# Kernel optimization log

Measured on AMD Instinct MI355X. Metric: run time of the kernel, lower is better.

The kernel has to match this reference:

```python
import jax, jax.numpy as jnp
import numpy as np

LN_EPS = 1e-5

def _layernorm(x, g, b):
    mu = x.mean(-1, keepdims=True)
    var = ((x - mu) ** 2).mean(-1, keepdims=True)
    return (x - mu) * jax.lax.rsqrt(var + LN_EPS) * g + b

def setup_inputs() -> dict:
    key = jax.random.key(0)
    ks = jax.random.split(key, 5)
    B, S, H, V = 1, 1024, 768, 50257
    return {
        "hidden_states": jax.random.normal(ks[0], (B, S, H), jnp.float32),
        "attention_mask": jnp.ones((B, S), jnp.int32),
        "alpha": jnp.float32(0.1),
        "ln_gamma": jnp.ones((H,), jnp.float32),
        "ln_beta": jnp.zeros((H,), jnp.float32),
        "W1": jax.random.normal(ks[1], (H, H), jnp.float32) * 0.02,
        "b1": jnp.zeros((H,), jnp.float32),
        "W2": jax.random.normal(ks[2], (H, H), jnp.float32) * 0.02,
        "b2": jnp.zeros((H,), jnp.float32),
        "lm_head_w": jax.random.normal(ks[3], (V, H), jnp.float32) * 0.02,
        "n_processors": 4,
        "k_steps": 4,
    }

def reference(hidden_states, attention_mask, alpha, ln_gamma, ln_beta,
              W1, b1, W2, b2, lm_head_w, n_processors, k_steps):
    P = int(n_processors)
    K = int(k_steps)
    mask = attention_mask.astype(hidden_states.dtype)[..., None]        # [B,S,1]
    # processor_states: [P,B,S,H] (all initialized to the same hidden state)
    states = jnp.broadcast_to(hidden_states[None], (P,) + hidden_states.shape)
    for _ in range(K):
        # eval mode: dropout=identity, no noise -> mutate == mask multiply
        mut = states * mask                                             # [P,B,S,H]
        if P > 1:
            # mean of other processors = (sum_all - self)/(P-1)
            observe = (mut.sum(0, keepdims=True) - mut) / (P - 1)
        else:
            observe = jnp.zeros_like(mut)
        merged = mut + alpha * observe
        normed = _layernorm(merged, ln_gamma, ln_beta)
        h = jax.nn.gelu(jnp.einsum('pbsh,ih->pbsi', normed, W1) + b1,
                        approximate=False)
        delta = jnp.einsum('pbsi,hi->pbsh', h, W2) + b2
        states = (mut + delta) * mask
    consensus = states.mean(0)                                          # [B,S,H]
    logits = jnp.einsum('bsh,vh->bsv', consensus, lm_head_w)            # [B,S,V]
    processor_logits = jnp.einsum('pbsh,vh->pbsv', states, lm_head_w)   # [P,B,S,V]
    return logits, processor_logits, states
```

## Files before the change

kernel.cpp:

```cpp
#include <hip/hip_runtime.h>
#include <hip/hip_bf16.h>
#include <math.h>

#define S_LEN 1024
#define HDIM  768
#define NPROC 4
#define VOCAB 50257
#define KSTEPS 4
#define LOOP_BLOCKS 96

typedef __attribute__((ext_vector_type(4))) float f32x4;
typedef __attribute__((ext_vector_type(8))) short bf16x8;
typedef __attribute__((ext_vector_type(4))) short short4v;

static __device__ __forceinline__ ushort f2bf(float f) {
  union { __hip_bfloat16 b; ushort u; } cv;
  cv.b = __float2bfloat16(f);
  return cv.u;
}

#define GLOAD16(gp, lp) __builtin_amdgcn_global_load_lds( \
    (const __attribute__((address_space(1))) unsigned int*)(gp), \
    (__attribute__((address_space(3))) unsigned int*)(lp), 16, 0, 0)

__global__ void prep_weights(const float* __restrict__ lmw, const float* __restrict__ W1,
                             const float* __restrict__ W2, ushort* __restrict__ lm_bf,
                             ushort* __restrict__ w1_bf, ushort* __restrict__ w2_bf) {
  const int LM4 = VOCAB * HDIM / 4;
  const int W4  = HDIM * HDIM / 4;
  const int LMB = (LM4 + 255) / 256;
  const int WB  = (W4 + 255) / 256;
  const int bid = blockIdx.x;
  const float* in; ushort* out; int n4, i;
  if (bid < LMB)           { in = lmw; out = lm_bf; n4 = LM4; i = bid * 256 + threadIdx.x; }
  else if (bid < LMB + WB) { in = W1;  out = w1_bf; n4 = W4;  i = (bid - LMB) * 256 + threadIdx.x; }
  else                     { in = W2;  out = w2_bf; n4 = W4;  i = (bid - LMB - WB) * 256 + threadIdx.x; }
  if (i >= n4) return;
  f32x4 v = ((const f32x4*)in)[i];
  short4v o;
#pragma unroll
  for (int j = 0; j < 4; j++) o[j] = (short)f2bf(v[j]);
  ((short4v*)out)[i] = o;
}

__global__ __launch_bounds__(256) void bcast_logits(
    const float* __restrict__ src, float* __restrict__ dst) {
  const size_t n4 = (size_t)S_LEN * VOCAB / 4;
  for (size_t i = (size_t)blockIdx.x * 256 + threadIdx.x; i < n4;
       i += (size_t)gridDim.x * 256) {
    f32x4 v = ((const f32x4*)src)[i];
#pragma unroll
    for (int p = 0; p < NPROC; p++)
      ((f32x4*)dst)[(size_t)p * n4 + i] = v;
  }
}

static __device__ __forceinline__ void grid_barrier(int* cnt, int target) {
  __syncthreads();
  if (threadIdx.x == 0) {
    __threadfence();
    atomicAdd(cnt, 1);
    while (atomicAdd(cnt, 0) < target) { }
    __threadfence();
  }
  __syncthreads();
}

template <int MODE>
static __device__ __forceinline__ void mlp_phase(
    const ushort* __restrict__ A, const ushort* __restrict__ B,
    const float* __restrict__ bias, ushort* __restrict__ out_bf,
    const float* __restrict__ src, float* __restrict__ dst,
    const int* __restrict__ mask,
    ushort lsA[][4096], ushort lsB[][2048]) {
  const int tid = threadIdx.x;
  const int bx = blockIdx.x;
  const int mt = bx & 7;
  const int nt = bx >> 3;
  const int wv = tid >> 6, lane = tid & 63;
  const int wm = wv >> 1, wn = wv & 1;
  const int g = lane >> 4, lr = lane & 15;

  f32x4 acc[4][2];
#pragma unroll
  for (int i = 0; i < 4; i++)
#pragma unroll
    for (int j = 0; j < 2; j++) acc[i][j] = (f32x4){0.f, 0.f, 0.f, 0.f};

  const int koff = (tid & 3) * 8;
  const int arow0 = mt * 128 + (tid >> 2);
  const ushort* gA0 = A + (size_t)arow0 * HDIM + koff;
  const ushort* gA1 = gA0 + (size_t)64 * HDIM;
  const ushort* gB0 = B + (size_t)(nt * 64 + (tid >> 2)) * HDIM + koff;
  const int dstl = (tid >> 2) * 32 + (tid & 3) * 8;

#define STAGE(kt, buf) do {                      \
    const int o_ = (kt) * 32;                    \
    GLOAD16(gA0 + o_, &lsA[buf][dstl]);          \
    GLOAD16(gA1 + o_, &lsA[buf][2048 + dstl]);   \
    GLOAD16(gB0 + o_, &lsB[buf][dstl]);          \
  } while (0)

  constexpr int NT = HDIM / 32;
  STAGE(0, 0);
  STAGE(1, 1);
  int cur = 0;
  for (int kt = 0; kt < NT; ++kt) {
    if (kt < NT - 1) asm volatile("s_waitcnt vmcnt(3)" ::: "memory");
    else             asm volatile("s_waitcnt vmcnt(0)" ::: "memory");
    __builtin_amdgcn_s_barrier();
    __builtin_amdgcn_sched_barrier(0);
    bf16x8 af[4], bfr[2];
#pragma unroll
    for (int mi = 0; mi < 4; mi++)
      af[mi] = *(const bf16x8*)(&lsA[cur][(wm * 64 + mi * 16 + lr) * 32 + g * 8]);
#pragma unroll
    for (int ni = 0; ni < 2; ni++)
      bfr[ni] = *(const bf16x8*)(&lsB[cur][(wn * 32 + ni * 16 + lr) * 32 + g * 8]);
    asm volatile("s_waitcnt lgkmcnt(0)" ::: "memory");
    __builtin_amdgcn_sched_barrier(0);
    __builtin_amdgcn_s_setprio(1);
#pragma unroll
    for (int mi = 0; mi < 4; mi++)
#pragma unroll
      for (int ni = 0; ni < 2; ni++)
        acc[mi][ni] = __builtin_amdgcn_mfma_f32_16x16x32_bf16(af[mi], bfr[ni], acc[mi][ni], 0, 0, 0);
    __builtin_amdgcn_s_setprio(0);
    __builtin_amdgcn_s_barrier();
    __builtin_amdgcn_sched_barrier(0);
    if (kt + 2 < NT) STAGE(kt + 2, cur);
    cur ^= 1;
  }
#undef STAGE

#pragma unroll
  for (int mi = 0; mi < 4; mi++) {
    const int mrow = mt * 128 + wm * 64 + mi * 16 + g * 4;
#pragma unroll
    for (int ni = 0; ni < 2; ni++) {
      const int ncol = nt * 64 + wn * 32 + ni * 16 + lr;
      const float bv = bias[ncol];
      if (MODE == 0) {
#pragma unroll
        for (int j = 0; j < 4; j++) {
          float x = acc[mi][ni][j] + bv;
          float ge = 0.5f * x * (1.f + erff(x * 0.70710678118654752f));
          out_bf[(size_t)(mrow + j) * HDIM + ncol] = f2bf(ge);
        }
      } else {
#pragma unroll
        for (int j = 0; j < 4; j++) {
          const int m = mrow + j;
          const float mk = (float)mask[m];
          const size_t idx = (size_t)m * HDIM + ncol;
          const float mut = src[idx] * mk;
          const float ns = (mut + acc[mi][ni][j] + bv) * mk;
          dst[idx] = ns;
          if (out_bf) out_bf[idx] = f2bf(ns);
        }
      }
    }
  }
}

__global__ __launch_bounds__(256) void fused_loop(
    const float* __restrict__ hidden, const int* __restrict__ mask,
    const float* __restrict__ alphap, const float* __restrict__ gamma,
    const float* __restrict__ beta,
    const ushort* __restrict__ w1, const float* __restrict__ b1,
    const ushort* __restrict__ w2, const float* __restrict__ b2,
    float* __restrict__ st1, ushort* __restrict__ nrm, ushort* __restrict__ hbuf,
    ushort* __restrict__ a_bf, float* __restrict__ states, int* __restrict__ cnt) {
  __shared__ __align__(16) ushort lsA[2][4096];
  __shared__ __align__(16) ushort lsB[2][2048];
  __shared__ float rs_[4], rq_[4];
  const int tid = threadIdx.x;
  const float a1 = 1.0f + alphap[0];
  int gen = 0;

  for (int k = 0; k < KSTEPS; k++) {
    const float* src = (k == 0) ? hidden : st1;
    for (int s = blockIdx.x; s < S_LEN; s += LOOP_BLOCKS) {
      const float mk = (float)mask[s];
      float merged[3];
      float lsum = 0.f, lsq = 0.f;
#pragma unroll
      for (int e = 0; e < 3; e++) {
        const int h = tid + e * 256;
        float mg = src[(size_t)s * HDIM + h] * mk * a1;
        merged[e] = mg;
        lsum += mg;
        lsq += mg * mg;
      }
#pragma unroll
      for (int off = 32; off > 0; off >>= 1) {
        lsum += __shfl_down(lsum, off, 64);
        lsq  += __shfl_down(lsq, off, 64);
      }
      const int wv = tid >> 6, ln = tid & 63;
      if (ln == 0) { rs_[wv] = lsum; rq_[wv] = lsq; }
      __syncthreads();
      const float ts = rs_[0] + rs_[1] + rs_[2] + rs_[3];
      const float tq = rq_[0] + rq_[1] + rq_[2] + rq_[3];
      const float mu = ts * (1.f / HDIM);
      const float var = tq * (1.f / HDIM) - mu * mu;
      const float rstd = rsqrtf(var + 1e-5f);
#pragma unroll
      for (int e = 0; e < 3; e++) {
        const int h = tid + e * 256;
        float nv = (merged[e] - mu) * rstd * gamma[h] + beta[h];
        nrm[(size_t)s * HDIM + h] = f2bf(nv);
      }
      __syncthreads();
    }
    grid_barrier(cnt, (++gen) * LOOP_BLOCKS);
    mlp_phase<0>(nrm, w1, b1, hbuf, nullptr, nullptr, mask, lsA, lsB);
    grid_barrier(cnt, (++gen) * LOOP_BLOCKS);
    mlp_phase<1>(hbuf, w2, b2, (k == KSTEPS - 1) ? a_bf : nullptr, src, st1, mask, lsA, lsB);
    grid_barrier(cnt, (++gen) * LOOP_BLOCKS);
  }
  for (int i = blockIdx.x * 256 + tid; i < S_LEN * HDIM / 4; i += LOOP_BLOCKS * 256) {
    f32x4 v = ((const f32x4*)st1)[i];
#pragma unroll
    for (int p = 0; p < NPROC; p++)
      ((f32x4*)states)[(size_t)p * (S_LEN * HDIM / 4) + i] = v;
  }
}

__global__ __launch_bounds__(512, 2) void gemm_lm(
    const ushort* __restrict__ A, const ushort* __restrict__ B,
    float* __restrict__ logits, int nrowsB) {
  __shared__ __align__(16) ushort lds[2][4][8192];
  ushort* ldsb = &lds[0][0][0];
  const int tid = threadIdx.x;
  const int bx = blockIdx.x;
  const int mt = bx & 3;
  const int nt = bx >> 2;
  const int wv = tid >> 6, lane = tid & 63;
  const int wm = wv >> 2, wn = wv & 3;
  const int g = lane >> 4, lr = lane & 15;

  f32x4 acc[8][4];
#pragma unroll
  for (int i = 0; i < 8; i++)
#pragma unroll
    for (int j = 0; j < 4; j++) acc[i][j] = (f32x4){0.f, 0.f, 0.f, 0.f};

  const ushort* gsrc[4][2];
#pragma unroll
  for (int j = 0; j < 2; j++) {
    const int c = j * 512 + wv * 64 + lane;
    const int qa = c >> 9, ra = (c >> 3) & 63, oa = (c & 7) ^ (ra & 7);
    gsrc[0][j] = A + (size_t)(mt * 256 + qa * 128 + ra) * HDIM + oa * 8;
    gsrc[1][j] = A + (size_t)(mt * 256 + qa * 128 + 64 + ra) * HDIM + oa * 8;
    const int qb = c >> 8, rb = (c >> 3) & 31, ob = (c & 7) ^ (rb & 7);
    int r2 = nt * 256 + qb * 64 + rb;      if (r2 >= nrowsB) r2 = nrowsB - 1;
    int r3 = nt * 256 + qb * 64 + 32 + rb; if (r3 >= nrowsB) r3 = nrowsB - 1;
    gsrc[2][j] = B + (size_t)r2 * HDIM + ob * 8;
    gsrc[3][j] = B + (size_t)r3 * HDIM + ob * 8;
  }
  const int a_lane = wm * 4096 + lr * 64;
  const int b_lane = wn * 2048 + lr * 64;
  int slot8[2];
  slot8[0] = ((0 + g) ^ (lr & 7)) * 8;
  slot8[1] = ((4 + g) ^ (lr & 7)) * 8;

#define STG(R_, tt_) do {                                                     \
    ushort* dst_ = ldsb + (size_t)((((tt_) & 1) * 4 + (R_)) * 8192 + wv * 512); \
    GLOAD16(gsrc[R_][0] + (size_t)(tt_) * 64, dst_);                          \
    GLOAD16(gsrc[R_][1] + (size_t)(tt_) * 64, dst_ + 4096);                   \
  } while (0)

#define MFMA_Q(MB, NB, AV, BV) do {                                           \
    __builtin_amdgcn_s_setprio(1);                                           \
    _Pragma("unroll")                                                        \
    for (int mi = 0; mi < 4; mi++)                                           \
      _Pragma("unroll")                                                      \
      for (int ni = 0; ni < 2; ni++)                                         \
        _Pragma("unroll")                                                    \
        for (int ks = 0; ks < 2; ks++)                                       \
          acc[(MB) + mi][(NB) + ni] = __builtin_amdgcn_mfma_f32_16x16x32_bf16( \
              AV[mi][ks], BV[ni][ks], acc[(MB) + mi][(NB) + ni], 0, 0, 0);   \
    __builtin_amdgcn_s_setprio(0);                                           \
  } while (0)

  constexpr int NT = HDIM / 64;
  STG(0, 0); STG(2, 0); STG(3, 0); STG(1, 0);
  asm volatile("s_waitcnt vmcnt(4)" ::: "memory");
  __builtin_amdgcn_sched_barrier(0);
  __builtin_amdgcn_s_barrier();

  bf16x8 af[4][2], blo[2][2], bhi[2][2];
  for (int t = 0; t < NT - 1; ++t) {
    const ushort* cp = ldsb + (size_t)(t & 1) * 32768;
#pragma unroll
    for (int mi = 0; mi < 4; mi++)
#pragma unroll
      for (int ks = 0; ks < 2; ks++)
        af[mi][ks] = *(const bf16x8*)(cp + a_lane + mi * 1024 + slot8[ks]);
#pragma unroll
    for (int ni = 0; ni < 2; ni++)
#pragma unroll
      for (int ks = 0; ks < 2; ks++)
        blo[ni][ks] = *(const bf16x8*)(cp + 16384 + b_lane + ni * 1024 + slot8[ks]);
    STG(0, t + 1);
    __builtin_amdgcn_s_barrier();
    asm volatile("s_waitcnt lgkmcnt(0)" ::: "memory");
    __builtin_amdgcn_sched_barrier(0);
    MFMA_Q(0, 0, af, blo);
    asm volatile("s_waitcnt vmcnt(4)" ::: "memory");
    __builtin_amdgcn_sched_barrier(0);
    __builtin_amdgcn_s_barrier();
#pragma unroll
    for (int ni = 0; ni < 2; ni++)
#pragma unroll
      for (int ks = 0; ks < 2; ks++)
        bhi[ni][ks] = *(const bf16x8*)(cp + 24576 + b_lane + ni * 1024 + slot8[ks]);
    STG(2, t + 1);
    __builtin_amdgcn_s_barrier();
    asm volatile("s_waitcnt lgkmcnt(0)" ::: "memory");
    __builtin_amdgcn_sched_barrier(0);
    MFMA_Q(0, 2, af, bhi);
    asm volatile("s_waitcnt vmcnt(4)" ::: "memory");
    __builtin_amdgcn_sched_barrier(0);
    __builtin_amdgcn_s_barrier();
#pragma unroll
    for (int mi = 0; mi < 4; mi++)
#pragma unroll
      for (int ks = 0; ks < 2; ks++)
        af[mi][ks] = *(const bf16x8*)(cp + 8192 + a_lane + mi * 1024 + slot8[ks]);
    STG(3, t + 1);
    __builtin_amdgcn_s_barrier();
    asm volatile("s_waitcnt lgkmcnt(0)" ::: "memory");
    __builtin_amdgcn_sched_barrier(0);
    MFMA_Q(4, 2, af, bhi);
    __builtin_amdgcn_s_barrier();
    STG(1, t + 1);
    __builtin_amdgcn_s_barrier();
    MFMA_Q(4, 0, af, blo);
    asm volatile("s_waitcnt vmcnt(4)" ::: "memory");
    __builtin_amdgcn_sched_barrier(0);
    __builtin_amdgcn_s_barrier();
  }
  {
    const int t = NT - 1;
    const ushort* cp = ldsb + (size_t)(t & 1) * 32768;
#pragma unroll
    for (int mi = 0; mi < 4; mi++)
#pragma unroll
      for (int ks = 0; ks < 2; ks++)
        af[mi][ks] = *(const bf16x8*)(cp + a_lane + mi * 1024 + slot8[ks]);
#pragma unroll
    for (int ni = 0; ni < 2; ni++)
#pragma unroll
      for (int ks = 0; ks < 2; ks++)
        blo[ni][ks] = *(const bf16x8*)(cp + 16384 + b_lane + ni * 1024 + slot8[ks]);
    __builtin_amdgcn_s_barrier();
    asm volatile("s_waitcnt lgkmcnt(0)" ::: "memory");
    __builtin_amdgcn_sched_barrier(0);
    MFMA_Q(0, 0, af, blo);
    asm volatile("s_waitcnt vmcnt(2)" ::: "memory");
    __builtin_amdgcn_sched_barrier(0);
    __builtin_amdgcn_s_barrier();
#pragma unroll
    for (int ni = 0; ni < 2; ni++)
#pragma unroll
      for (int ks = 0; ks < 2; ks++)
        bhi[ni][ks] = *(const bf16x8*)(cp + 24576 + b_lane + ni * 1024 + slot8[ks]);
    __builtin_amdgcn_s_barrier();
    asm volatile("s_waitcnt lgkmcnt(0)" ::: "memory");
    __builtin_amdgcn_sched_barrier(0);
    MFMA_Q(0, 2, af, bhi);
    asm volatile("s_waitcnt vmcnt(0)" ::: "memory");
    __builtin_amdgcn_sched_barrier(0);
    __builtin_amdgcn_s_barrier();
#pragma unroll
    for (int mi = 0; mi < 4; mi++)
#pragma unroll
      for (int ks = 0; ks < 2; ks++)
        af[mi][ks] = *(const bf16x8*)(cp + 8192 + a_lane + mi * 1024 + slot8[ks]);
    asm volatile("s_waitcnt lgkmcnt(0)" ::: "memory");
    __builtin_amdgcn_sched_barrier(0);
    MFMA_Q(4, 2, af, bhi);
    MFMA_Q(4, 0, af, blo);
  }
#undef STG
#undef MFMA_Q

  float* sc = ((float*)ldsb) + wv * 1024;
  const int ncol0 = nt * 256 + wn * 64;
  const bool fast = (ncol0 + 64) <= nrowsB;
#pragma unroll
  for (int mi = 0; mi < 8; mi++) {
    __syncthreads();
#pragma unroll
    for (int ni = 0; ni < 4; ni++)
#pragma unroll
      for (int j = 0; j < 4; j++)
        sc[(g * 4 + j) * 64 + ni * 16 + lr] = acc[mi][ni][j];
    __syncthreads();
    const int srow0 = mt * 256 + wm * 128 + mi * 16;
    const int c0 = ncol0 + lr * 4;
#pragma unroll
    for (int jj = 0; jj < 4; jj++) {
      const f32x4 v = *(const f32x4*)&sc[(g * 4 + jj) * 64 + lr * 4];
      const int s = srow0 + g * 4 + jj;
      if (fast) {
        *(f32x4*)&logits[(size_t)s * VOCAB + c0] = v;
      } else {
#pragma unroll
        for (int cc = 0; cc < 4; cc++)
          if (c0 + cc < nrowsB) logits[(size_t)s * VOCAB + c0 + cc] = v[cc];
      }
    }
  }
}

extern "C" void kernel_launch(void* const* d_in, const int* in_sizes, int n_in,
                              void* d_out, int out_size, void* d_ws, size_t ws_size,
                              hipStream_t stream) {
  const float* hidden = (const float*)d_in[0];
  const int*   mask   = (const int*)d_in[1];
  const float* alphap = (const float*)d_in[2];
  const float* gamma  = (const float*)d_in[3];
  const float* beta   = (const float*)d_in[4];
  const float* W1     = (const float*)d_in[5];
  const float* b1     = (const float*)d_in[6];
  const float* W2     = (const float*)d_in[7];
  const float* b2     = (const float*)d_in[8];
  const float* lmw    = (const float*)d_in[9];

  float* logits  = (float*)d_out;
  float* plogits = logits + (size_t)S_LEN * VOCAB;
  float* states  = plogits + (size_t)NPROC * S_LEN * VOCAB;

  uint8_t* ws = (uint8_t*)d_ws;
  ushort* lm_bf  = (ushort*)ws;
  ushort* w1_bf  = (ushort*)(ws + 77194752);
  ushort* w2_bf  = (ushort*)(ws + 78374400);
  ushort* nrm_bf = (ushort*)(ws + 79554048);
  ushort* h_bf   = (ushort*)(ws + 81126912);
  ushort* a_bf   = (ushort*)(ws + 82699776);
  float*  st1    = (float*) (ws + 84272640);
  int*    cnt    = (int*)   (ws + 87418368);
  if (ws_size < 87418496) return;

  hipMemsetAsync(cnt, 0, 128, stream);
  const int LMB = (VOCAB * HDIM / 4 + 255) / 256, WB = (HDIM * HDIM / 4 + 255) / 256;
  prep_weights<<<LMB + 2 * WB, 256, 0, stream>>>(lmw, W1, W2, lm_bf, w1_bf, w2_bf);
  fused_loop<<<LOOP_BLOCKS, 256, 0, stream>>>(
      hidden, mask, alphap, gamma, beta, w1_bf, b1, w2_bf, b2,
      st1, nrm_bf, h_bf, a_bf, states, cnt);
  gemm_lm<<<((VOCAB + 255) / 256) * 4, 512, 0, stream>>>(a_bf, lm_bf, logits, VOCAB);
  bcast_logits<<<2048, 256, 0, stream>>>(logits, plogits);
}
```

Before: 664.1 us.

## Replace persistent grid-barrier loop kernel with separate per-step kernel launches

The persistent fused_loop kernel, which ran on 96 blocks and synchronised through atomic grid barriers, is split into three kernels launched per step: a layernorm kernel with one block per row, and two MLP GEMM kernels. This removes the spin-wait barriers and lets the layernorm use 1024 blocks instead of 96. The final broadcast of states into the four processor copies moves into the last GEMM epilogue. The cost is 12 extra kernel launches and the loss of on-chip continuity between phases.

```diff
diff --git a/kernel.cpp b/kernel.cpp
--- a/kernel.cpp
+++ b/kernel.cpp
@@ -7,7 +7,6 @@
 #define NPROC 4
 #define VOCAB 50257
 #define KSTEPS 4
-#define LOOP_BLOCKS 96
 
 typedef __attribute__((ext_vector_type(4))) float f32x4;
 typedef __attribute__((ext_vector_type(8))) short bf16x8;
@@ -55,24 +54,54 @@
   }
 }
 
-static __device__ __forceinline__ void grid_barrier(int* cnt, int target) {
+__global__ __launch_bounds__(256) void merge_ln_p1(
+    const float* __restrict__ src, const int* __restrict__ mask,
+    const float* __restrict__ alphap, const float* __restrict__ gamma,
+    const float* __restrict__ beta, ushort* __restrict__ normed) {
+  const int s = blockIdx.x;
+  const int tid = threadIdx.x;
+  const float mk = (float)mask[s];
+  const float a1 = 1.0f + alphap[0];
+  float merged[3];
+  float lsum = 0.f, lsq = 0.f;
+#pragma unroll
+  for (int e = 0; e < 3; e++) {
+    const int h = tid + e * 256;
+    float mg = src[(size_t)s * HDIM + h] * mk * a1;
+    merged[e] = mg;
+    lsum += mg;
+    lsq += mg * mg;
+  }
+#pragma unroll
+  for (int off = 32; off > 0; off >>= 1) {
+    lsum += __shfl_down(lsum, off, 64);
+    lsq  += __shfl_down(lsq, off, 64);
+  }
+  __shared__ float rs_[4], rq_[4];
+  const int wv = tid >> 6, ln = tid & 63;
+  if (ln == 0) { rs_[wv] = lsum; rq_[wv] = lsq; }
   __syncthreads();
-  if (threadIdx.x == 0) {
-    __threadfence();
-    atomicAdd(cnt, 1);
-    while (atomicAdd(cnt, 0) < target) { }
-    __threadfence();
-  }
-  __syncthreads();
+  const float ts = rs_[0] + rs_[1] + rs_[2] + rs_[3];
+  const float tq = rq_[0] + rq_[1] + rq_[2] + rq_[3];
+  const float mu = ts * (1.f / HDIM);
+  const float var = tq * (1.f / HDIM) - mu * mu;
+  const float rstd = rsqrtf(var + 1e-5f);
+#pragma unroll
+  for (int e = 0; e < 3; e++) {
+    const int h = tid + e * 256;
+    float nv = (merged[e] - mu) * rstd * gamma[h] + beta[h];
+    normed[(size_t)s * HDIM + h] = f2bf(nv);
+  }
 }
 
 template <int MODE>
-static __device__ __forceinline__ void mlp_phase(
+__global__ __launch_bounds__(256, 4) void gemm_mlp(
     const ushort* __restrict__ A, const ushort* __restrict__ B,
     const float* __restrict__ bias, ushort* __restrict__ out_bf,
     const float* __restrict__ src, float* __restrict__ dst,
-    const int* __restrict__ mask,
-    ushort lsA[][4096], ushort lsB[][2048]) {
+    float* __restrict__ states, const int* __restrict__ mask) {
+  __shared__ __align__(16) ushort lsA[2][4096];
+  __shared__ __align__(16) ushort lsB[2][2048];
   const int tid = threadIdx.x;
   const int bx = blockIdx.x;
   const int mt = bx & 7;
@@ -155,75 +184,17 @@
           const size_t idx = (size_t)m * HDIM + ncol;
           const float mut = src[idx] * mk;
           const float ns = (mut + acc[mi][ni][j] + bv) * mk;
-          dst[idx] = ns;
-          if (out_bf) out_bf[idx] = f2bf(ns);
+          if (out_bf) {
+            out_bf[idx] = f2bf(ns);
+#pragma unroll
+            for (int p = 0; p < NPROC; p++)
+              states[(size_t)p * S_LEN * HDIM + idx] = ns;
+          } else {
+            dst[idx] = ns;
+          }
         }
       }
     }
-  }
-}
-
-__global__ __launch_bounds__(256) void fused_loop(
-    const float* __restrict__ hidden, const int* __restrict__ mask,
-    const float* __restrict__ alphap, const float* __restrict__ gamma,
-    const float* __restrict__ beta,
-    const ushort* __restrict__ w1, const float* __restrict__ b1,
-    const ushort* __restrict__ w2, const float* __restrict__ b2,
-    float* __restrict__ st1, ushort* __restrict__ nrm, ushort* __restrict__ hbuf,
-    ushort* __restrict__ a_bf, float* __restrict__ states, int* __restrict__ cnt) {
-  __shared__ __align__(16) ushort lsA[2][4096];
-  __shared__ __align__(16) ushort lsB[2][2048];
-  __shared__ float rs_[4], rq_[4];
-  const int tid = threadIdx.x;
-  const float a1 = 1.0f + alphap[0];
-  int gen = 0;
-
-  for (int k = 0; k < KSTEPS; k++) {
-    const float* src = (k == 0) ? hidden : st1;
-    for (int s = blockIdx.x; s < S_LEN; s += LOOP_BLOCKS) {
-      const float mk = (float)mask[s];
-      float merged[3];
-      float lsum = 0.f, lsq = 0.f;
-#pragma unroll
-      for (int e = 0; e < 3; e++) {
-        const int h = tid + e * 256;
-        float mg = src[(size_t)s * HDIM + h] * mk * a1;
-        merged[e] = mg;
-        lsum += mg;
-        lsq += mg * mg;
-      }
-#pragma unroll
-      for (int off = 32; off > 0; off >>= 1) {
-        lsum += __shfl_down(lsum, off, 64);
-        lsq  += __shfl_down(lsq, off, 64);
-      }
-      const int wv = tid >> 6, ln = tid & 63;
-      if (ln == 0) { rs_[wv] = lsum; rq_[wv] = lsq; }
-      __syncthreads();
-      const float ts = rs_[0] + rs_[1] + rs_[2] + rs_[3];
-      const float tq = rq_[0] + rq_[1] + rq_[2] + rq_[3];
-      const float mu = ts * (1.f / HDIM);
-      const float var = tq * (1.f / HDIM) - mu * mu;
-      const float rstd = rsqrtf(var + 1e-5f);
-#pragma unroll
-      for (int e = 0; e < 3; e++) {
-        const int h = tid + e * 256;
-        float nv = (merged[e] - mu) * rstd * gamma[h] + beta[h];
-        nrm[(size_t)s * HDIM + h] = f2bf(nv);
-      }
-      __syncthreads();
-    }
-    grid_barrier(cnt, (++gen) * LOOP_BLOCKS);
-    mlp_phase<0>(nrm, w1, b1, hbuf, nullptr, nullptr, mask, lsA, lsB);
-    grid_barrier(cnt, (++gen) * LOOP_BLOCKS);
-    mlp_phase<1>(hbuf, w2, b2, (k == KSTEPS - 1) ? a_bf : nullptr, src, st1, mask, lsA, lsB);
-    grid_barrier(cnt, (++gen) * LOOP_BLOCKS);
-  }
-  for (int i = blockIdx.x * 256 + tid; i < S_LEN * HDIM / 4; i += LOOP_BLOCKS * 256) {
-    f32x4 v = ((const f32x4*)st1)[i];
-#pragma unroll
-    for (int p = 0; p < NPROC; p++)
-      ((f32x4*)states)[(size_t)p * (S_LEN * HDIM / 4) + i] = v;
   }
 }
 
@@ -442,15 +413,20 @@
   ushort* h_bf   = (ushort*)(ws + 81126912);
   ushort* a_bf   = (ushort*)(ws + 82699776);
   float*  st1    = (float*) (ws + 84272640);
-  int*    cnt    = (int*)   (ws + 87418368);
-  if (ws_size < 87418496) return;
-
-  hipMemsetAsync(cnt, 0, 128, stream);
+  if (ws_size < 87418368) return;
+
   const int LMB = (VOCAB * HDIM / 4 + 255) / 256, WB = (HDIM * HDIM / 4 + 255) / 256;
   prep_weights<<<LMB + 2 * WB, 256, 0, stream>>>(lmw, W1, W2, lm_bf, w1_bf, w2_bf);
-  fused_loop<<<LOOP_BLOCKS, 256, 0, stream>>>(
-      hidden, mask, alphap, gamma, beta, w1_bf, b1, w2_bf, b2,
-      st1, nrm_bf, h_bf, a_bf, states, cnt);
+
+  for (int k = 0; k < KSTEPS; k++) {
+    const float* src = (k == 0) ? hidden : st1;
+    merge_ln_p1<<<S_LEN, 256, 0, stream>>>(src, mask, alphap, gamma, beta, nrm_bf);
+    gemm_mlp<0><<<(HDIM / 64) * 8, 256, 0, stream>>>(
+        nrm_bf, w1_bf, b1, h_bf, nullptr, nullptr, nullptr, mask);
+    gemm_mlp<1><<<(HDIM / 64) * 8, 256, 0, stream>>>(
+        h_bf, w2_bf, b2, (k == KSTEPS - 1) ? (ushort*)a_bf : nullptr,
+        src, st1, states, mask);
+  }
   gemm_lm<<<((VOCAB + 255) / 256) * 4, 512, 0, stream>>>(a_bf, lm_bf, logits, VOCAB);
   bcast_logits<<<2048, 256, 0, stream>>>(logits, plogits);
 }
```

New measurement: 540.3 us, median of 2. 1.23x faster.
